# Optimization experiments

Hardware: AMD Instinct MI355X
Metric: run time of the kernel (lower is better)

Reference implementation:

```python
import jax, jax.numpy as jnp
import numpy as np

L = 3        # number of GatedGCN layers
N = 30000    # nodes
E = 480000   # edges (avg degree 16)
D = 128      # hidden dim (= in_dim = out_dim)
IN = 128     # input feature dim
G = 64       # graphs in batch
C = 10       # classes


def setup_inputs() -> dict:
    key = jax.random.key(0)
    ks = jax.random.split(key, 32)
    s = 0.05  # weight scale to keep activations / sigmoid gates in a sane range
    inp = {
        "h": jax.random.normal(ks[0], (N, IN), jnp.float32),
        "e": jax.random.normal(ks[1], (E, IN), jnp.float32),
        "snorm_n": jax.random.uniform(ks[2], (N, 1), jnp.float32),
        "snorm_e": jax.random.uniform(ks[3], (E, 1), jnp.float32),
        "src": jax.random.randint(ks[4], (E,), 0, N, jnp.int32),
        "dst": jax.random.randint(ks[5], (E,), 0, N, jnp.int32),
        "graph_id": jnp.sort(jax.random.randint(ks[6], (N,), 0, G, jnp.int32)),
        # input embeddings
        "Wh_emb": jax.random.normal(ks[7], (IN, D), jnp.float32) * s,
        "bh_emb": jnp.zeros((D,), jnp.float32),
        "We_emb": jax.random.normal(ks[8], (IN, D), jnp.float32) * s,
        "be_emb": jnp.zeros((D,), jnp.float32),
        # per-layer A,B,C,D,E linears (stacked over L)
        "WA": jax.random.normal(ks[9], (L, D, D), jnp.float32) * s,
        "bA": jnp.zeros((L, D), jnp.float32),
        "WB": jax.random.normal(ks[10], (L, D, D), jnp.float32) * s,
        "bB": jnp.zeros((L, D), jnp.float32),
        "WC": jax.random.normal(ks[11], (L, D, D), jnp.float32) * s,
        "bC": jnp.zeros((L, D), jnp.float32),
        "WD": jax.random.normal(ks[12], (L, D, D), jnp.float32) * s,
        "bD": jnp.zeros((L, D), jnp.float32),
        "WE": jax.random.normal(ks[13], (L, D, D), jnp.float32) * s,
        "bE": jnp.zeros((L, D), jnp.float32),
        # batch-norm affine params (node / edge)
        "gn_h": jnp.ones((L, D), jnp.float32),
        "bt_h": jnp.zeros((L, D), jnp.float32),
        "gn_e": jnp.ones((L, D), jnp.float32),
        "bt_e": jnp.zeros((L, D), jnp.float32),
        # readout linear
        "Wr": jax.random.normal(ks[14], (D, C), jnp.float32) * s,
        "br": jnp.zeros((C,), jnp.float32),
    }
    return inp


def _bn(x, gamma, beta):
    # training-mode BatchNorm1d: biased batch stats over the node/edge axis
    mu = jnp.mean(x, axis=0)
    var = jnp.var(x, axis=0)
    return (x - mu) * jax.lax.rsqrt(var + 1e-5) * gamma + beta


def reference(h, e, snorm_n, snorm_e, src, dst, graph_id,
              Wh_emb, bh_emb, We_emb, be_emb,
              WA, bA, WB, bB, WC, bC, WD, bD, WE, bE,
              gn_h, bt_h, gn_e, bt_e, Wr, br):
    n_nodes = h.shape[0]
    h = h @ Wh_emb + bh_emb
    e = e @ We_emb + be_emb
    for l in range(WA.shape[0]):
        h_in, e_in = h, e
        Ah = h @ WA[l] + bA[l]
        Bh = h @ WB[l] + bB[l]
        Dh = h @ WD[l] + bD[l]
        Eh = h @ WE[l] + bE[l]
        Ce = e @ WC[l] + bC[l]
        # message: e_ij = Ce + Dh_src + Eh_dst ; gate = sigmoid(e_ij)
        e_new = Ce + Dh[src] + Eh[dst]                       # [E, D]
        sig = jax.nn.sigmoid(e_new)
        # reduce at dst: gated weighted mean of Bh_src
        num = jax.ops.segment_sum(sig * Bh[src], dst, num_segments=n_nodes)
        den = jax.ops.segment_sum(sig, dst, num_segments=n_nodes)
        h_new = Ah + num / (den + 1e-6)
        # graph norm
        h_new = h_new * snorm_n
        e_new = e_new * snorm_e
        # batch norm + ReLU + residual (dropout p=0 -> identity)
        h_new = jax.nn.relu(_bn(h_new, gn_h[l], bt_h[l]))
        e_new = jax.nn.relu(_bn(e_new, gn_e[l], bt_e[l]))
        h = h_in + h_new
        e = e_in + e_new
    # mean_nodes readout per graph, then linear classifier
    sums = jax.ops.segment_sum(h, graph_id, num_segments=G)
    cnt = jax.ops.segment_sum(jnp.ones((n_nodes, 1), h.dtype), graph_id, num_segments=G)
    hg = sums / jnp.maximum(cnt, 1.0)
    return hg @ Wr + br
```

## Files before the change

### kernel.cpp

```cpp
#include <hip/hip_runtime.h>
#include <cstdint>
#include <cstddef>

#define N_NODES  30000
#define N_EDGES  480000
#define N_LAYERS 3
#define N_GRAPHS 64
#define N_CLASS  10
#define NREP     32

typedef __attribute__((ext_vector_type(8))) short short8v;
typedef __attribute__((ext_vector_type(4))) float f32x4;

__device__ __forceinline__ unsigned short f2bf(float x) {
  union { float f; unsigned u; } v; v.f = x;
  unsigned r = v.u + 0x7FFFu + ((v.u >> 16) & 1u);
  return (unsigned short)(r >> 16);
}
__device__ __forceinline__ float bf2f(unsigned short h) {
  union { unsigned u; float f; } v; v.u = ((unsigned)h) << 16;
  return v.f;
}
__device__ __forceinline__ int swzW(int row, int off16) {
  return (row << 8) | (off16 ^ ((row & 7) << 4));
}

__global__ void wconv(const float* __restrict__ Wh, const float* __restrict__ We,
                      const float* __restrict__ WA, const float* __restrict__ WB,
                      const float* __restrict__ WC, const float* __restrict__ WD,
                      const float* __restrict__ WE, unsigned short* __restrict__ Wt)
{
  const int mi  = blockIdx.x >> 6;
  const int idx = (blockIdx.x & 63) * 256 + threadIdx.x;
  const float* src;
  if      (mi == 0) src = Wh;
  else if (mi == 1) src = We;
  else if (mi < 5)  src = WA + (size_t)(mi - 2) * 16384;
  else if (mi < 8)  src = WB + (size_t)(mi - 5) * 16384;
  else if (mi < 11) src = WC + (size_t)(mi - 8) * 16384;
  else if (mi < 14) src = WD + (size_t)(mi - 11) * 16384;
  else              src = WE + (size_t)(mi - 14) * 16384;
  const int k = idx >> 7, n = idx & 127;
  Wt[(size_t)mi * 16384 + (size_t)n * 128 + k] = f2bf(src[idx]);
}

struct GemmArgs {
  const unsigned short* Wt[4];
  const float* bias[4];
  unsigned short* out[4];
};

template<int NMAT, bool AFP32, bool APPLY>
__global__ __launch_bounds__(256)
void gemm_mm(const void* __restrict__ Ap, GemmArgs g, int M,
             const float* __restrict__ tb, const float2* __restrict__ pqh,
             unsigned short* __restrict__ hout)
{
  __shared__ __align__(16) unsigned char WL[32768];
  unsigned short* Wl = (unsigned short*)WL;
  const int t = threadIdx.x;
  const int w = t >> 6, l = t & 63;
  const int lr = l & 15, lkb = (l >> 4) * 8;
  const int r0 = blockIdx.x * 64;
  const bool vrow = (r0 + w * 16 + lr) < M;
  int arow = r0 + w * 16 + lr; if (arow >= M) arow = M - 1;

  short8v a[4];
  if (AFP32) {
    const float* A = (const float*)Ap;
#pragma unroll
    for (int kk = 0; kk < 4; ++kk) {
      const float* p = A + (size_t)arow * 128 + kk * 32 + lkb;
      const float4 u = *(const float4*)p;
      const float4 v = *(const float4*)(p + 4);
      short8v av;
      av[0]=f2bf(u.x); av[1]=f2bf(u.y); av[2]=f2bf(u.z); av[3]=f2bf(u.w);
      av[4]=f2bf(v.x); av[5]=f2bf(v.y); av[6]=f2bf(v.z); av[7]=f2bf(v.w);
      a[kk] = av;
    }
  } else if (APPLY) {
    const unsigned short* A = (const unsigned short*)Ap;
#pragma unroll
    for (int kk = 0; kk < 4; ++kk) {
      const float* tp = tb + (size_t)arow * 128 + kk * 32 + lkb;
      const float4 t0 = *(const float4*)tp;
      const float4 t1 = *(const float4*)(tp + 4);
      const short8v hr = *(const short8v*)(A + (size_t)arow * 128 + kk * 32 + lkb);
      const float tt[8] = {t0.x,t0.y,t0.z,t0.w,t1.x,t1.y,t1.z,t1.w};
      short8v av;
#pragma unroll
      for (int j = 0; j < 8; ++j) {
        const float2 PQ = pqh[kk * 32 + lkb + j];
        const float x = tt[j] * PQ.x + PQ.y;
        av[j] = (short)f2bf(bf2f((unsigned short)hr[j]) + fmaxf(x, 0.f));
      }
      a[kk] = av;
      if (vrow) *(short8v*)(hout + (size_t)arow * 128 + kk * 32 + lkb) = av;
    }
  } else {
    const unsigned short* A = (const unsigned short*)Ap;
#pragma unroll
    for (int kk = 0; kk < 4; ++kk)
      a[kk] = *(const short8v*)(A + (size_t)arow * 128 + kk * 32 + lkb);
  }

#pragma unroll
  for (int m = 0; m < NMAT; ++m) {
    if (m) __syncthreads();
#pragma unroll
    for (int p = 0; p < 8; ++p) {
      const int ci = t + p * 256;
      *(short8v*)(WL + swzW(ci >> 4, (ci & 15) * 16)) = *(const short8v*)(g.Wt[m] + (size_t)ci * 8);
    }
    __syncthreads();
    f32x4 acc[8];
#pragma unroll
    for (int ct = 0; ct < 8; ++ct) acc[ct] = (f32x4){0.f, 0.f, 0.f, 0.f};
#pragma unroll
    for (int kk = 0; kk < 4; ++kk)
#pragma unroll
      for (int ct = 0; ct < 8; ++ct) {
        const short8v b = *(const short8v*)(WL + swzW(ct * 16 + lr, kk * 64 + (l >> 4) * 16));
        acc[ct] = __builtin_amdgcn_mfma_f32_16x16x32_bf16(a[kk], b, acc[ct], 0, 0, 0);
      }
    __syncthreads();
#pragma unroll
    for (int ct = 0; ct < 8; ++ct) {
      const float bb = g.bias[m][ct * 16 + lr];
#pragma unroll
      for (int q = 0; q < 4; ++q)
        Wl[(w * 16 + (l >> 4) * 4 + q) * 136 + ct * 16 + lr] = f2bf(acc[ct][q] + bb);
    }
    __syncthreads();
    unsigned short* out = g.out[m];
#pragma unroll
    for (int p = 0; p < 4; ++p) {
      const int ci = t + p * 256;
      const int rr = ci >> 4, co = (ci & 15) * 8;
      const int grow = r0 + rr;
      if (grow < M)
        *(short8v*)(out + (size_t)grow * 128 + co) = *(const short8v*)(Wl + rr * 136 + co);
    }
  }
}

template<int LMODE>
__global__ __launch_bounds__(256)
void edge_kern(const void* __restrict__ Ap, unsigned short* __restrict__ eres,
               unsigned short* __restrict__ enew,
               const unsigned short* __restrict__ Wt, const float* __restrict__ bias,
               const unsigned short* __restrict__ Dh, const unsigned short* __restrict__ Eh,
               const int* __restrict__ src, const int* __restrict__ dst,
               const float* __restrict__ snorm_e, const float2* __restrict__ pq)
{
  __shared__ __align__(16) unsigned char SM[33792];
  __shared__ float2 pql[128];
  unsigned short* TB = (unsigned short*)SM;
  const int t = threadIdx.x;
  const int w = t >> 6, l = t & 63;
  const int lr = l & 15, lkb = (l >> 4) * 8;
  const int r0 = blockIdx.x * 128;
  if (LMODE >= 2 && t < 128) pql[t] = pq[t];
#pragma unroll
  for (int p = 0; p < 8; ++p) {
    const int ci = t + p * 256;
    *(short8v*)(SM + swzW(ci >> 4, (ci & 15) * 16)) = *(const short8v*)(Wt + (size_t)ci * 8);
  }

  short8v a[2][4];
  if (LMODE == 0) {
    const float* A = (const float*)Ap;
#pragma unroll
    for (int mt = 0; mt < 2; ++mt) {
      const int arow = r0 + w * 32 + mt * 16 + lr;
#pragma unroll
      for (int kk = 0; kk < 4; ++kk) {
        const float* p2 = A + (size_t)arow * 128 + kk * 32 + lkb;
        const float4 u = *(const float4*)p2;
        const float4 v = *(const float4*)(p2 + 4);
        short8v av;
        av[0]=f2bf(u.x); av[1]=f2bf(u.y); av[2]=f2bf(u.z); av[3]=f2bf(u.w);
        av[4]=f2bf(v.x); av[5]=f2bf(v.y); av[6]=f2bf(v.z); av[7]=f2bf(v.w);
        a[mt][kk] = av;
      }
    }
  } else if (LMODE == 1) {
    const unsigned short* A = (const unsigned short*)Ap;
#pragma unroll
    for (int mt = 0; mt < 2; ++mt) {
      const int arow = r0 + w * 32 + mt * 16 + lr;
#pragma unroll
      for (int kk = 0; kk < 4; ++kk)
        a[mt][kk] = *(const short8v*)(A + (size_t)arow * 128 + kk * 32 + lkb);
    }
  }
  __syncthreads();

  if (LMODE >= 2) {
    const unsigned short* A = (const unsigned short*)Ap;
#pragma unroll
    for (int mt = 0; mt < 2; ++mt) {
      const int arow = r0 + w * 32 + mt * 16 + lr;
      const float sn = snorm_e[arow];
#pragma unroll
      for (int kk = 0; kk < 4; ++kk) {
        const short8v ep = *(const short8v*)(enew + (size_t)arow * 128 + kk * 32 + lkb);
        const short8v er = *(const short8v*)(A + (size_t)arow * 128 + kk * 32 + lkb);
        short8v av;
#pragma unroll
        for (int j = 0; j < 8; ++j) {
          const float2 PQ = pql[kk * 32 + lkb + j];
          const float x = bf2f((unsigned short)ep[j]) * sn * PQ.x + PQ.y;
          av[j] = (short)f2bf(bf2f((unsigned short)er[j]) + fmaxf(x, 0.f));
        }
        a[mt][kk] = av;
        if (LMODE == 2)
          *(short8v*)(eres + (size_t)arow * 128 + kk * 32 + lkb) = av;
      }
    }
  }

  f32x4 acc[2][8];
#pragma unroll
  for (int mt = 0; mt < 2; ++mt)
#pragma unroll
    for (int ct = 0; ct < 8; ++ct) acc[mt][ct] = (f32x4){0.f, 0.f, 0.f, 0.f};
#pragma unroll
  for (int kk = 0; kk < 4; ++kk)
#pragma unroll
    for (int ct = 0; ct < 8; ++ct) {
      const short8v b = *(const short8v*)(SM + swzW(ct * 16 + lr, kk * 64 + (l >> 4) * 16));
      acc[0][ct] = __builtin_amdgcn_mfma_f32_16x16x32_bf16(a[0][kk], b, acc[0][ct], 0, 0, 0);
      acc[1][ct] = __builtin_amdgcn_mfma_f32_16x16x32_bf16(a[1][kk], b, acc[1][ct], 0, 0, 0);
    }
  __syncthreads();
#pragma unroll
  for (int ct = 0; ct < 8; ++ct) {
    const float bb = bias[ct * 16 + lr];
#pragma unroll
    for (int mt = 0; mt < 2; ++mt)
#pragma unroll
      for (int q = 0; q < 4; ++q)
        TB[(w * 32 + mt * 16 + (l >> 4) * 4 + q) * 132 + ct * 16 + lr] = f2bf(acc[mt][ct][q] + bb);
  }
  __syncthreads();
#pragma unroll
  for (int p = 0; p < 8; ++p) {
    const int ci = t + p * 256;
    const int rr = ci >> 4, co = (ci & 15) * 8;
    const int edge = r0 + rr;
    const short8v ce = *(const short8v*)(TB + rr * 132 + co);
    if (LMODE == 0) {
      *(short8v*)(eres + (size_t)edge * 128 + co) = ce;
    } else {
      const int s = src[edge], d = dst[edge];
      const short8v dv = *(const short8v*)(Dh + (size_t)s * 128 + co);
      const short8v ev = *(const short8v*)(Eh + (size_t)d * 128 + co);
      short8v ov;
#pragma unroll
      for (int j = 0; j < 8; ++j)
        ov[j] = (short)f2bf(bf2f((unsigned short)ce[j]) + bf2f((unsigned short)dv[j]) + bf2f((unsigned short)ev[j]));
      *(short8v*)(enew + (size_t)edge * 128 + co) = ov;
    }
  }
}

__global__ void hist_kernel(const int* __restrict__ dst, int* __restrict__ cnt, int E)
{
  const int i = blockIdx.x * 256 + threadIdx.x;
  if (i < E) atomicAdd(&cnt[dst[i]], 1);
}

__global__ void scan_kernel(const int* __restrict__ cnt, int* __restrict__ start,
                            int* __restrict__ cursor, int n, int total)
{
  __shared__ int lds[1024];
  const int tid = threadIdx.x;
  const int chunk = (n + 1023) / 1024;
  const int lo = tid * chunk, hi = min(lo + chunk, n);
  int s = 0;
  for (int i = lo; i < hi; ++i) s += cnt[i];
  lds[tid] = s;
  __syncthreads();
  for (int off = 1; off < 1024; off <<= 1) {
    const int v = (tid >= off) ? lds[tid - off] : 0;
    __syncthreads();
    lds[tid] += v;
    __syncthreads();
  }
  int run = (tid == 0) ? 0 : lds[tid - 1];
  for (int i = lo; i < hi; ++i) { start[i] = run; cursor[i] = run; run += cnt[i]; }
  if (tid == 0) start[n] = total;
}

__global__ void scatter_kernel(const int* __restrict__ dst, const int* __restrict__ src,
                               const float* __restrict__ sne, int* __restrict__ cursor,
                               int* __restrict__ csr, int* __restrict__ csrc,
                               float* __restrict__ csne, int E)
{
  const int i = blockIdx.x * 256 + threadIdx.x;
  if (i < E) {
    const int p = atomicAdd(&cursor[dst[i]], 1);
    csr[p] = i; csrc[p] = src[i]; csne[p] = sne[i];
  }
}

__global__ __launch_bounds__(256)
void aggregate(const unsigned short* __restrict__ enew, const unsigned short* __restrict__ Bh,
               const unsigned short* __restrict__ Ah, const float* __restrict__ snorm_n,
               const int* __restrict__ start, const int* __restrict__ csr,
               const int* __restrict__ csrc, const float* __restrict__ csne,
               float* __restrict__ tbuf, float* __restrict__ statrep, int doE)
{
  __shared__ float2 red[16][132];
  const int t = threadIdx.x;
  const int g = t >> 4, q = t & 15;
  const int v = blockIdx.x * 16 + g;
  const int s0 = start[v], s1 = start[v + 1];
  float num[8] = {0,0,0,0,0,0,0,0}, den[8] = {0,0,0,0,0,0,0,0};
  float psE[8] = {0,0,0,0,0,0,0,0}, pqE[8] = {0,0,0,0,0,0,0,0};

  float sn = 0.f;
  short8v ev = {}, bv = {};
  if (s0 < s1) {
    const int eid = csr[s0];
    sn = csne[s0];
    ev = *(const short8v*)(enew + (size_t)eid * 128 + q * 8);
    bv = *(const short8v*)(Bh + (size_t)csrc[s0] * 128 + q * 8);
  }
  for (int i = s0; i < s1; ++i) {
    float snn = 0.f;
    short8v evn = {}, bvn = {};
    if (i + 1 < s1) {
      const int eid = csr[i + 1];
      snn = csne[i + 1];
      evn = *(const short8v*)(enew + (size_t)eid * 128 + q * 8);
      bvn = *(const short8v*)(Bh + (size_t)csrc[i + 1] * 128 + q * 8);
    }
#pragma unroll
    for (int j = 0; j < 8; ++j) {
      const float en = bf2f((unsigned short)ev[j]);
      const float sg = 1.f / (1.f + __expf(-en));
      num[j] = fmaf(sg, bf2f((unsigned short)bv[j]), num[j]);
      den[j] += sg;
      if (doE) { const float tv = en * sn; psE[j] += tv; pqE[j] = fmaf(tv, tv, pqE[j]); }
    }
    ev = evn; bv = bvn; sn = snn;
  }
  const float snv = snorm_n[v];
  const short8v av = *(const short8v*)(Ah + (size_t)v * 128 + q * 8);
  float hv[8];
#pragma unroll
  for (int j = 0; j < 8; ++j)
    hv[j] = (bf2f((unsigned short)av[j]) + num[j] / (den[j] + 1e-6f)) * snv;
  *(float4*)(tbuf + (size_t)v * 128 + q * 8)     = make_float4(hv[0], hv[1], hv[2], hv[3]);
  *(float4*)(tbuf + (size_t)v * 128 + q * 8 + 4) = make_float4(hv[4], hv[5], hv[6], hv[7]);

  float* rep = statrep + (size_t)(blockIdx.x & (NREP - 1)) * 512;
#pragma unroll
  for (int j = 0; j < 8; ++j) red[g][q * 8 + j] = make_float2(hv[j], hv[j] * hv[j]);
  __syncthreads();
  if (t < 128) {
    float s = 0.f, qq = 0.f;
    for (int gg = 0; gg < 16; ++gg) { s += red[gg][t].x; qq += red[gg][t].y; }
    atomicAdd(rep + t, s); atomicAdd(rep + 128 + t, qq);
  }
  if (doE) {
    __syncthreads();
#pragma unroll
    for (int j = 0; j < 8; ++j) red[g][q * 8 + j] = make_float2(psE[j], pqE[j]);
    __syncthreads();
    if (t < 128) {
      float s = 0.f, qq = 0.f;
      for (int gg = 0; gg < 16; ++gg) { s += red[gg][t].x; qq += red[gg][t].y; }
      atomicAdd(rep + 256 + t, s); atomicAdd(rep + 384 + t, qq);
    }
  }
}

__global__ void finalize_kernel(float* __restrict__ rep, float2* __restrict__ pqh,
                                float2* __restrict__ pqe,
                                const float* __restrict__ gn_h_l, const float* __restrict__ bt_h_l,
                                const float* __restrict__ gn_e_l, const float* __restrict__ bt_e_l,
                                float invN, float invE, int doE)
{
  const int c = threadIdx.x;
  float sH = 0.f, qH = 0.f, sE = 0.f, qE = 0.f;
  for (int r = 0; r < NREP; ++r) {
    float* p = rep + (size_t)r * 512;
    sH += p[c]; qH += p[128 + c]; sE += p[256 + c]; qE += p[384 + c];
    p[c] = 0.f; p[128 + c] = 0.f; p[256 + c] = 0.f; p[384 + c] = 0.f;
  }
  const float muH = sH * invN;
  const float vH  = fmaxf(qH * invN - muH * muH, 0.f);
  const float PH  = rsqrtf(vH + 1e-5f) * gn_h_l[c];
  pqh[c] = make_float2(PH, bt_h_l[c] - muH * PH);
  if (doE) {
    const float muE = sE * invE;
    const float vE  = fmaxf(qE * invE - muE * muE, 0.f);
    const float PE  = rsqrtf(vE + 1e-5f) * gn_e_l[c];
    pqe[c] = make_float2(PE, bt_e_l[c] - muE * PE);
  }
}

__global__ void readout_scatter(const unsigned short* __restrict__ h, const float* __restrict__ tb,
                                const float2* __restrict__ pqh, const int* __restrict__ gid,
                                float* __restrict__ gsum, int* __restrict__ gcnt, int N)
{
  const int c = threadIdx.x;
  const float2 PQ = pqh[c];
  const int row0 = blockIdx.x * 256;
  int cur = -1, cnt = 0;
  float s = 0.f;
  for (int r = 0; r < 256; ++r) {
    const int v = row0 + r;
    if (v >= N) break;
    const int g = gid[v];
    if (g != cur) {
      if (cur >= 0) {
        atomicAdd(&gsum[(size_t)cur * 128 + c], s);
        if (c == 0) atomicAdd(&gcnt[cur], cnt);
      }
      cur = g; s = 0.f; cnt = 0;
    }
    s += bf2f(h[(size_t)v * 128 + c]) + fmaxf(tb[(size_t)v * 128 + c] * PQ.x + PQ.y, 0.f);
    ++cnt;
  }
  if (cur >= 0) {
    atomicAdd(&gsum[(size_t)cur * 128 + c], s);
    if (c == 0) atomicAdd(&gcnt[cur], cnt);
  }
}

__global__ void readout_final(const float* __restrict__ gsum, const int* __restrict__ gcnt,
                              const float* __restrict__ Wr, const float* __restrict__ br,
                              float* __restrict__ out)
{
  const int g = blockIdx.x;
  const int t = threadIdx.x;
  __shared__ float hg[128];
  const float cnt = fmaxf((float)gcnt[g], 1.f);
  hg[t] = gsum[(size_t)g * 128 + t] / cnt;
  __syncthreads();
  if (t < N_CLASS) {
    float acc = br[t];
    for (int k = 0; k < 128; ++k) acc = fmaf(hg[k], Wr[k * N_CLASS + t], acc);
    out[g * N_CLASS + t] = acc;
  }
}

extern "C" void kernel_launch(void* const* d_in, const int* in_sizes, int n_in,
                              void* d_out, int out_size, void* d_ws, size_t ws_size,
                              hipStream_t stream)
{
  const float* h_in    = (const float*)d_in[0];
  const float* e_in    = (const float*)d_in[1];
  const float* snorm_n = (const float*)d_in[2];
  const float* snorm_e = (const float*)d_in[3];
  const int*   src     = (const int*)d_in[4];
  const int*   dst     = (const int*)d_in[5];
  const int*   gid     = (const int*)d_in[6];
  const float* Wh_emb  = (const float*)d_in[7];
  const float* bh_emb  = (const float*)d_in[8];
  const float* We_emb  = (const float*)d_in[9];
  const float* be_emb  = (const float*)d_in[10];
  const float* WA = (const float*)d_in[11]; const float* bA = (const float*)d_in[12];
  const float* WB = (const float*)d_in[13]; const float* bB = (const float*)d_in[14];
  const float* WC = (const float*)d_in[15]; const float* bC = (const float*)d_in[16];
  const float* WD = (const float*)d_in[17]; const float* bD = (const float*)d_in[18];
  const float* WE = (const float*)d_in[19]; const float* bE = (const float*)d_in[20];
  const float* gn_h = (const float*)d_in[21]; const float* bt_h = (const float*)d_in[22];
  const float* gn_e = (const float*)d_in[23]; const float* bt_e = (const float*)d_in[24];
  const float* Wr = (const float*)d_in[25]; const float* br = (const float*)d_in[26];
  float* out = (float*)d_out;
  (void)in_sizes; (void)n_in; (void)out_size; (void)ws_size;

  char* ws = (char*)d_ws;
  size_t off = 0;
  auto alloc = [&](size_t bytes) -> char* {
    off = (off + 255) & ~(size_t)255;
    char* p = ws + off;
    off += bytes;
    return p;
  };
  const size_t ND = (size_t)N_NODES * 128, ED = (size_t)N_EDGES * 128;
  unsigned short* hbuf = (unsigned short*)alloc(ND * 2);
  unsigned short* ebuf = (unsigned short*)alloc(ED * 2);
  unsigned short* enew = (unsigned short*)alloc(ED * 2);
  unsigned short* Ah   = (unsigned short*)alloc(ND * 2);
  unsigned short* Bh   = (unsigned short*)alloc(ND * 2);
  unsigned short* Dh   = (unsigned short*)alloc(ND * 2);
  unsigned short* Eh   = (unsigned short*)alloc(ND * 2);
  float* tbuf          = (float*)alloc(ND * 4);
  unsigned short* Wt   = (unsigned short*)alloc((size_t)17 * 16384 * 2);
  float* statrep       = (float*)alloc((size_t)NREP * 512 * 4);
  float2* pqh          = (float2*)alloc(128 * 8);
  float2* pqe          = (float2*)alloc(128 * 8);
  int* cnt    = (int*)alloc((size_t)N_NODES * 4);
  int* start  = (int*)alloc((size_t)(N_NODES + 1) * 4);
  int* cursor = (int*)alloc((size_t)N_NODES * 4);
  int* csr    = (int*)alloc((size_t)N_EDGES * 4);
  int* csrc   = (int*)alloc((size_t)N_EDGES * 4);
  float* csne = (float*)alloc((size_t)N_EDGES * 4);
  float* gsum = (float*)alloc((size_t)N_GRAPHS * 128 * 4);
  int* gcnt   = (int*)alloc((size_t)N_GRAPHS * 4);

  wconv<<<17 * 64, 256, 0, stream>>>(Wh_emb, We_emb, WA, WB, WC, WD, WE, Wt);

  hipMemsetAsync(cnt, 0, (size_t)N_NODES * 4, stream);
  hipMemsetAsync(statrep, 0, (size_t)NREP * 512 * 4, stream);
  hist_kernel<<<(N_EDGES + 255) / 256, 256, 0, stream>>>(dst, cnt, N_EDGES);
  scan_kernel<<<1, 1024, 0, stream>>>(cnt, start, cursor, N_NODES, N_EDGES);
  scatter_kernel<<<(N_EDGES + 255) / 256, 256, 0, stream>>>(dst, src, snorm_e, cursor,
                                                            csr, csrc, csne, N_EDGES);

  const int gbN = (N_NODES + 63) / 64;
  const int gbE = N_EDGES / 128;

  {
    GemmArgs g{};
    g.Wt[0] = Wt + 0 * 16384; g.bias[0] = bh_emb; g.out[0] = hbuf;
    gemm_mm<1, true, false><<<gbN, 256, 0, stream>>>(h_in, g, N_NODES, nullptr, nullptr, nullptr);
  }
  edge_kern<0><<<gbE, 256, 0, stream>>>(e_in, ebuf, nullptr, Wt + 1 * 16384, be_emb,
                                        nullptr, nullptr, nullptr, nullptr, nullptr, nullptr);

  for (int l = 0; l < N_LAYERS; ++l) {
    const size_t bOff = (size_t)l * 128;
    const int doE = (l < N_LAYERS - 1) ? 1 : 0;
    {
      GemmArgs g{};
      g.Wt[0] = Wt + (size_t)(2 + l)  * 16384; g.bias[0] = bA + bOff; g.out[0] = Ah;
      g.Wt[1] = Wt + (size_t)(5 + l)  * 16384; g.bias[1] = bB + bOff; g.out[1] = Bh;
      g.Wt[2] = Wt + (size_t)(11 + l) * 16384; g.bias[2] = bD + bOff; g.out[2] = Dh;
      g.Wt[3] = Wt + (size_t)(14 + l) * 16384; g.bias[3] = bE + bOff; g.out[3] = Eh;
      if (l == 0)
        gemm_mm<4, false, false><<<gbN, 256, 0, stream>>>(hbuf, g, N_NODES, nullptr, nullptr, nullptr);
      else
        gemm_mm<4, false, true><<<gbN, 256, 0, stream>>>(hbuf, g, N_NODES, tbuf, pqh, hbuf);
    }
    const unsigned short* WtC = Wt + (size_t)(8 + l) * 16384;
    if (l == 0)
      edge_kern<1><<<gbE, 256, 0, stream>>>(ebuf, nullptr, enew, WtC, bC + bOff,
                                            Dh, Eh, src, dst, nullptr, nullptr);
    else if (l == 1)
      edge_kern<2><<<gbE, 256, 0, stream>>>(ebuf, ebuf, enew, WtC, bC + bOff,
                                            Dh, Eh, src, dst, snorm_e, pqe);
    else
      edge_kern<3><<<gbE, 256, 0, stream>>>(ebuf, nullptr, enew, WtC, bC + bOff,
                                            Dh, Eh, src, dst, snorm_e, pqe);
    aggregate<<<N_NODES / 16, 256, 0, stream>>>(enew, Bh, Ah, snorm_n,
                                                start, csr, csrc, csne, tbuf, statrep, doE);
    finalize_kernel<<<1, 128, 0, stream>>>(statrep, pqh, pqe, gn_h + bOff, bt_h + bOff,
                                           gn_e + bOff, bt_e + bOff,
                                           1.f / N_NODES, 1.f / N_EDGES, doE);
  }

  hipMemsetAsync(gsum, 0, (size_t)N_GRAPHS * 128 * 4 + (size_t)N_GRAPHS * 4, stream);
  readout_scatter<<<(N_NODES + 255) / 256, 128, 0, stream>>>(hbuf, tbuf, pqh, gid, gsum, gcnt, N_NODES);
  readout_final<<<N_GRAPHS, 128, 0, stream>>>(gsum, gcnt, Wr, br, out);
}
```

Before: 984.9 us.

## Fuse BN finalize into aggregate, store node pre-norm in bf16, shrink edge tiles

```diff
diff --git a/kernel.cpp b/kernel.cpp
--- a/kernel.cpp
+++ b/kernel.cpp
@@ -53,7 +53,7 @@
 template<int NMAT, bool AFP32, bool APPLY>
 __global__ __launch_bounds__(256)
 void gemm_mm(const void* __restrict__ Ap, GemmArgs g, int M,
-             const float* __restrict__ tb, const float2* __restrict__ pqh,
+             const unsigned short* __restrict__ tb, const float2* __restrict__ pqh,
              unsigned short* __restrict__ hout)
 {
   __shared__ __align__(16) unsigned char WL[32768];
@@ -82,16 +82,13 @@
     const unsigned short* A = (const unsigned short*)Ap;
 #pragma unroll
     for (int kk = 0; kk < 4; ++kk) {
-      const float* tp = tb + (size_t)arow * 128 + kk * 32 + lkb;
-      const float4 t0 = *(const float4*)tp;
-      const float4 t1 = *(const float4*)(tp + 4);
+      const short8v tv = *(const short8v*)(tb + (size_t)arow * 128 + kk * 32 + lkb);
       const short8v hr = *(const short8v*)(A + (size_t)arow * 128 + kk * 32 + lkb);
-      const float tt[8] = {t0.x,t0.y,t0.z,t0.w,t1.x,t1.y,t1.z,t1.w};
       short8v av;
 #pragma unroll
       for (int j = 0; j < 8; ++j) {
         const float2 PQ = pqh[kk * 32 + lkb + j];
-        const float x = tt[j] * PQ.x + PQ.y;
+        const float x = bf2f((unsigned short)tv[j]) * PQ.x + PQ.y;
         av[j] = (short)f2bf(bf2f((unsigned short)hr[j]) + fmaxf(x, 0.f));
       }
       a[kk] = av;
@@ -153,13 +150,14 @@
                const int* __restrict__ src, const int* __restrict__ dst,
                const float* __restrict__ snorm_e, const float2* __restrict__ pq)
 {
-  __shared__ __align__(16) unsigned char SM[33792];
+  __shared__ __align__(16) unsigned char SM[32768];
   __shared__ float2 pql[128];
   unsigned short* TB = (unsigned short*)SM;
   const int t = threadIdx.x;
   const int w = t >> 6, l = t & 63;
   const int lr = l & 15, lkb = (l >> 4) * 8;
-  const int r0 = blockIdx.x * 128;
+  const int r0 = blockIdx.x * 64;
+  const int arow = r0 + w * 16 + lr;
   if (LMODE >= 2 && t < 128) pql[t] = pq[t];
 #pragma unroll
   for (int p = 0; p < 8; ++p) {
@@ -167,85 +165,68 @@
     *(short8v*)(SM + swzW(ci >> 4, (ci & 15) * 16)) = *(const short8v*)(Wt + (size_t)ci * 8);
   }
 
-  short8v a[2][4];
+  short8v a[4];
   if (LMODE == 0) {
     const float* A = (const float*)Ap;
 #pragma unroll
-    for (int mt = 0; mt < 2; ++mt) {
-      const int arow = r0 + w * 32 + mt * 16 + lr;
-#pragma unroll
-      for (int kk = 0; kk < 4; ++kk) {
-        const float* p2 = A + (size_t)arow * 128 + kk * 32 + lkb;
-        const float4 u = *(const float4*)p2;
-        const float4 v = *(const float4*)(p2 + 4);
-        short8v av;
-        av[0]=f2bf(u.x); av[1]=f2bf(u.y); av[2]=f2bf(u.z); av[3]=f2bf(u.w);
-        av[4]=f2bf(v.x); av[5]=f2bf(v.y); av[6]=f2bf(v.z); av[7]=f2bf(v.w);
-        a[mt][kk] = av;
-      }
+    for (int kk = 0; kk < 4; ++kk) {
+      const float* p2 = A + (size_t)arow * 128 + kk * 32 + lkb;
+      const float4 u = *(const float4*)p2;
+      const float4 v = *(const float4*)(p2 + 4);
+      short8v av;
+      av[0]=f2bf(u.x); av[1]=f2bf(u.y); av[2]=f2bf(u.z); av[3]=f2bf(u.w);
+      av[4]=f2bf(v.x); av[5]=f2bf(v.y); av[6]=f2bf(v.z); av[7]=f2bf(v.w);
+      a[kk] = av;
     }
   } else if (LMODE == 1) {
     const unsigned short* A = (const unsigned short*)Ap;
 #pragma unroll
-    for (int mt = 0; mt < 2; ++mt) {
-      const int arow = r0 + w * 32 + mt * 16 + lr;
-#pragma unroll
-      for (int kk = 0; kk < 4; ++kk)
-        a[mt][kk] = *(const short8v*)(A + (size_t)arow * 128 + kk * 32 + lkb);
-    }
+    for (int kk = 0; kk < 4; ++kk)
+      a[kk] = *(const short8v*)(A + (size_t)arow * 128 + kk * 32 + lkb);
   }
   __syncthreads();
 
   if (LMODE >= 2) {
     const unsigned short* A = (const unsigned short*)Ap;
-#pragma unroll
-    for (int mt = 0; mt < 2; ++mt) {
-      const int arow = r0 + w * 32 + mt * 16 + lr;
-      const float sn = snorm_e[arow];
-#pragma unroll
-      for (int kk = 0; kk < 4; ++kk) {
-        const short8v ep = *(const short8v*)(enew + (size_t)arow * 128 + kk * 32 + lkb);
-        const short8v er = *(const short8v*)(A + (size_t)arow * 128 + kk * 32 + lkb);
-        short8v av;
-#pragma unroll
-        for (int j = 0; j < 8; ++j) {
-          const float2 PQ = pql[kk * 32 + lkb + j];
-          const float x = bf2f((unsigned short)ep[j]) * sn * PQ.x + PQ.y;
-          av[j] = (short)f2bf(bf2f((unsigned short)er[j]) + fmaxf(x, 0.f));
-        }
-        a[mt][kk] = av;
-        if (LMODE == 2)
-          *(short8v*)(eres + (size_t)arow * 128 + kk * 32 + lkb) = av;
+    const float sn = snorm_e[arow];
+#pragma unroll
+    for (int kk = 0; kk < 4; ++kk) {
+      const short8v ep = *(const short8v*)(enew + (size_t)arow * 128 + kk * 32 + lkb);
+      const short8v er = *(const short8v*)(A + (size_t)arow * 128 + kk * 32 + lkb);
+      short8v av;
+#pragma unroll
+      for (int j = 0; j < 8; ++j) {
+        const float2 PQ = pql[kk * 32 + lkb + j];
+        const float x = bf2f((unsigned short)ep[j]) * sn * PQ.x + PQ.y;
+        av[j] = (short)f2bf(bf2f((unsigned short)er[j]) + fmaxf(x, 0.f));
       }
-    }
-  }
-
-  f32x4 acc[2][8];
-#pragma unroll
-  for (int mt = 0; mt < 2; ++mt)
-#pragma unroll
-    for (int ct = 0; ct < 8; ++ct) acc[mt][ct] = (f32x4){0.f, 0.f, 0.f, 0.f};
+      a[kk] = av;
+      if (LMODE == 2)
+        *(short8v*)(eres + (size_t)arow * 128 + kk * 32 + lkb) = av;
+    }
+  }
+
+  f32x4 acc[8];
+#pragma unroll
+  for (int ct = 0; ct < 8; ++ct) acc[ct] = (f32x4){0.f, 0.f, 0.f, 0.f};
 #pragma unroll
   for (int kk = 0; kk < 4; ++kk)
 #pragma unroll
     for (int ct = 0; ct < 8; ++ct) {
       const short8v b = *(const short8v*)(SM + swzW(ct * 16 + lr, kk * 64 + (l >> 4) * 16));
-      acc[0][ct] = __builtin_amdgcn_mfma_f32_16x16x32_bf16(a[0][kk], b, acc[0][ct], 0, 0, 0);
-      acc[1][ct] = __builtin_amdgcn_mfma_f32_16x16x32_bf16(a[1][kk], b, acc[1][ct], 0, 0, 0);
+      acc[ct] = __builtin_amdgcn_mfma_f32_16x16x32_bf16(a[kk], b, acc[ct], 0, 0, 0);
     }
   __syncthreads();
 #pragma unroll
   for (int ct = 0; ct < 8; ++ct) {
     const float bb = bias[ct * 16 + lr];
 #pragma unroll
-    for (int mt = 0; mt < 2; ++mt)
-#pragma unroll
-      for (int q = 0; q < 4; ++q)
-        TB[(w * 32 + mt * 16 + (l >> 4) * 4 + q) * 132 + ct * 16 + lr] = f2bf(acc[mt][ct][q] + bb);
-  }
-  __syncthreads();
-#pragma unroll
-  for (int p = 0; p < 8; ++p) {
+    for (int q = 0; q < 4; ++q)
+      TB[(w * 16 + (l >> 4) * 4 + q) * 132 + ct * 16 + lr] = f2bf(acc[ct][q] + bb);
+  }
+  __syncthreads();
+#pragma unroll
+  for (int p = 0; p < 4; ++p) {
     const int ci = t + p * 256;
     const int rr = ci >> 4, co = (ci & 15) * 8;
     const int edge = r0 + rr;
@@ -305,14 +286,19 @@
   }
 }
 
+template<int DOE>
 __global__ __launch_bounds__(256)
 void aggregate(const unsigned short* __restrict__ enew, const unsigned short* __restrict__ Bh,
                const unsigned short* __restrict__ Ah, const float* __restrict__ snorm_n,
                const int* __restrict__ start, const int* __restrict__ csr,
                const int* __restrict__ csrc, const float* __restrict__ csne,
-               float* __restrict__ tbuf, float* __restrict__ statrep, int doE)
+               unsigned short* __restrict__ tbuf, float* __restrict__ statrep,
+               int* __restrict__ ticket, float2* __restrict__ pqh, float2* __restrict__ pqe,
+               const float* __restrict__ gn_h_l, const float* __restrict__ bt_h_l,
+               const float* __restrict__ gn_e_l, const float* __restrict__ bt_e_l)
 {
   __shared__ float2 red[16][132];
+  __shared__ int lastF;
   const int t = threadIdx.x;
   const int g = t >> 4, q = t & 15;
   const int v = blockIdx.x * 16 + g;
@@ -343,18 +329,20 @@
       const float sg = 1.f / (1.f + __expf(-en));
       num[j] = fmaf(sg, bf2f((unsigned short)bv[j]), num[j]);
       den[j] += sg;
-      if (doE) { const float tv = en * sn; psE[j] += tv; pqE[j] = fmaf(tv, tv, pqE[j]); }
+      if (DOE) { const float tv = en * sn; psE[j] += tv; pqE[j] = fmaf(tv, tv, pqE[j]); }
     }
     ev = evn; bv = bvn; sn = snn;
   }
   const float snv = snorm_n[v];
   const short8v av = *(const short8v*)(Ah + (size_t)v * 128 + q * 8);
   float hv[8];
-#pragma unroll
-  for (int j = 0; j < 8; ++j)
+  short8v tout;
+#pragma unroll
+  for (int j = 0; j < 8; ++j) {
     hv[j] = (bf2f((unsigned short)av[j]) + num[j] / (den[j] + 1e-6f)) * snv;
-  *(float4*)(tbuf + (size_t)v * 128 + q * 8)     = make_float4(hv[0], hv[1], hv[2], hv[3]);
-  *(float4*)(tbuf + (size_t)v * 128 + q * 8 + 4) = make_float4(hv[4], hv[5], hv[6], hv[7]);
+    tout[j] = (short)f2bf(hv[j]);
+  }
+  *(short8v*)(tbuf + (size_t)v * 128 + q * 8) = tout;
 
   float* rep = statrep + (size_t)(blockIdx.x & (NREP - 1)) * 512;
 #pragma unroll
@@ -365,7 +353,7 @@
     for (int gg = 0; gg < 16; ++gg) { s += red[gg][t].x; qq += red[gg][t].y; }
     atomicAdd(rep + t, s); atomicAdd(rep + 128 + t, qq);
   }
-  if (doE) {
+  if (DOE) {
     __syncthreads();
 #pragma unroll
     for (int j = 0; j < 8; ++j) red[g][q * 8 + j] = make_float2(psE[j], pqE[j]);
@@ -376,34 +364,37 @@
       atomicAdd(rep + 256 + t, s); atomicAdd(rep + 384 + t, qq);
     }
   }
-}
-
-__global__ void finalize_kernel(float* __restrict__ rep, float2* __restrict__ pqh,
-                                float2* __restrict__ pqe,
-                                const float* __restrict__ gn_h_l, const float* __restrict__ bt_h_l,
-                                const float* __restrict__ gn_e_l, const float* __restrict__ bt_e_l,
-                                float invN, float invE, int doE)
-{
-  const int c = threadIdx.x;
-  float sH = 0.f, qH = 0.f, sE = 0.f, qE = 0.f;
-  for (int r = 0; r < NREP; ++r) {
-    float* p = rep + (size_t)r * 512;
-    sH += p[c]; qH += p[128 + c]; sE += p[256 + c]; qE += p[384 + c];
-    p[c] = 0.f; p[128 + c] = 0.f; p[256 + c] = 0.f; p[384 + c] = 0.f;
-  }
-  const float muH = sH * invN;
-  const float vH  = fmaxf(qH * invN - muH * muH, 0.f);
-  const float PH  = rsqrtf(vH + 1e-5f) * gn_h_l[c];
-  pqh[c] = make_float2(PH, bt_h_l[c] - muH * PH);
-  if (doE) {
-    const float muE = sE * invE;
-    const float vE  = fmaxf(qE * invE - muE * muE, 0.f);
-    const float PE  = rsqrtf(vE + 1e-5f) * gn_e_l[c];
-    pqe[c] = make_float2(PE, bt_e_l[c] - muE * PE);
-  }
-}
-
-__global__ void readout_scatter(const unsigned short* __restrict__ h, const float* __restrict__ tb,
+  __threadfence();
+  __syncthreads();
+  if (t == 0) lastF = (atomicAdd(ticket, 1) == (int)gridDim.x - 1) ? 1 : 0;
+  __syncthreads();
+  if (lastF) {
+    __threadfence();
+    if (t < 128) {
+      const int c = t;
+      float sH = 0.f, qH = 0.f, sE = 0.f, qE = 0.f;
+      for (int r = 0; r < NREP; ++r) {
+        volatile float* p = statrep + (size_t)r * 512;
+        sH += p[c]; qH += p[128 + c];
+        if (DOE) { sE += p[256 + c]; qE += p[384 + c]; }
+        p[c] = 0.f; p[128 + c] = 0.f; p[256 + c] = 0.f; p[384 + c] = 0.f;
+      }
+      const float invN = 1.f / N_NODES, invE = 1.f / N_EDGES;
+      const float muH = sH * invN;
+      const float vH  = fmaxf(qH * invN - muH * muH, 0.f);
+      const float PH  = rsqrtf(vH + 1e-5f) * gn_h_l[c];
+      pqh[c] = make_float2(PH, bt_h_l[c] - muH * PH);
+      if (DOE) {
+        const float muE = sE * invE;
+        const float vE  = fmaxf(qE * invE - muE * muE, 0.f);
+        const float PE  = rsqrtf(vE + 1e-5f) * gn_e_l[c];
+        pqe[c] = make_float2(PE, bt_e_l[c] - muE * PE);
+      }
+    }
+  }
+}
+
+__global__ void readout_scatter(const unsigned short* __restrict__ h, const unsigned short* __restrict__ tb,
                                 const float2* __restrict__ pqh, const int* __restrict__ gid,
                                 float* __restrict__ gsum, int* __restrict__ gcnt, int N)
 {
@@ -423,7 +414,7 @@
       }
       cur = g; s = 0.f; cnt = 0;
     }
-    s += bf2f(h[(size_t)v * 128 + c]) + fmaxf(tb[(size_t)v * 128 + c] * PQ.x + PQ.y, 0.f);
+    s += bf2f(h[(size_t)v * 128 + c]) + fmaxf(bf2f(tb[(size_t)v * 128 + c]) * PQ.x + PQ.y, 0.f);
     ++cnt;
   }
   if (cur >= 0) {
@@ -491,31 +482,34 @@
   unsigned short* Bh   = (unsigned short*)alloc(ND * 2);
   unsigned short* Dh   = (unsigned short*)alloc(ND * 2);
   unsigned short* Eh   = (unsigned short*)alloc(ND * 2);
-  float* tbuf          = (float*)alloc(ND * 4);
+  unsigned short* tbuf = (unsigned short*)alloc(ND * 2);
   unsigned short* Wt   = (unsigned short*)alloc((size_t)17 * 16384 * 2);
-  float* statrep       = (float*)alloc((size_t)NREP * 512 * 4);
   float2* pqh          = (float2*)alloc(128 * 8);
   float2* pqe          = (float2*)alloc(128 * 8);
-  int* cnt    = (int*)alloc((size_t)N_NODES * 4);
   int* start  = (int*)alloc((size_t)(N_NODES + 1) * 4);
   int* cursor = (int*)alloc((size_t)N_NODES * 4);
   int* csr    = (int*)alloc((size_t)N_EDGES * 4);
   int* csrc   = (int*)alloc((size_t)N_EDGES * 4);
   float* csne = (float*)alloc((size_t)N_EDGES * 4);
-  float* gsum = (float*)alloc((size_t)N_GRAPHS * 128 * 4);
-  int* gcnt   = (int*)alloc((size_t)N_GRAPHS * 4);
+  char* zbase = (char*)alloc(0);
+  int*   cnt     = (int*)alloc((size_t)N_NODES * 4);
+  float* statrep = (float*)alloc((size_t)NREP * 512 * 4);
+  float* gsum    = (float*)alloc((size_t)N_GRAPHS * 128 * 4);
+  int*   gcnt    = (int*)alloc((size_t)N_GRAPHS * 4);
+  int*   tickets = (int*)alloc(8 * 4);
+  char* zend = (char*)alloc(0);
+
+  hipMemsetAsync(zbase, 0, (size_t)(zend - zbase), stream);
 
   wconv<<<17 * 64, 256, 0, stream>>>(Wh_emb, We_emb, WA, WB, WC, WD, WE, Wt);
 
-  hipMemsetAsync(cnt, 0, (size_t)N_NODES * 4, stream);
-  hipMemsetAsync(statrep, 0, (size_t)NREP * 512 * 4, stream);
   hist_kernel<<<(N_EDGES + 255) / 256, 256, 0, stream>>>(dst, cnt, N_EDGES);
   scan_kernel<<<1, 1024, 0, stream>>>(cnt, start, cursor, N_NODES, N_EDGES);
   scatter_kernel<<<(N_EDGES + 255) / 256, 256, 0, stream>>>(dst, src, snorm_e, cursor,
                                                             csr, csrc, csne, N_EDGES);
 
   const int gbN = (N_NODES + 63) / 64;
-  const int gbE = N_EDGES / 128;
+  const int gbE = N_EDGES / 64;
 
   {
     GemmArgs g{};
@@ -527,7 +521,6 @@
 
   for (int l = 0; l < N_LAYERS; ++l) {
     const size_t bOff = (size_t)l * 128;
-    const int doE = (l < N_LAYERS - 1) ? 1 : 0;
     {
       GemmArgs g{};
       g.Wt[0] = Wt + (size_t)(2 + l)  * 16384; g.bias[0] = bA + bOff; g.out[0] = Ah;
@@ -549,14 +542,16 @@
     else
       edge_kern<3><<<gbE, 256, 0, stream>>>(ebuf, nullptr, enew, WtC, bC + bOff,
                                             Dh, Eh, src, dst, snorm_e, pqe);
-    aggregate<<<N_NODES / 16, 256, 0, stream>>>(enew, Bh, Ah, snorm_n,
-                                                start, csr, csrc, csne, tbuf, statrep, doE);
-    finalize_kernel<<<1, 128, 0, stream>>>(statrep, pqh, pqe, gn_h + bOff, bt_h + bOff,
-                                           gn_e + bOff, bt_e + bOff,
-                                           1.f / N_NODES, 1.f / N_EDGES, doE);
-  }
-
-  hipMemsetAsync(gsum, 0, (size_t)N_GRAPHS * 128 * 4 + (size_t)N_GRAPHS * 4, stream);
+    if (l < N_LAYERS - 1)
+      aggregate<1><<<N_NODES / 16, 256, 0, stream>>>(enew, Bh, Ah, snorm_n, start, csr, csrc, csne,
+                                                     tbuf, statrep, tickets + l, pqh, pqe,
+                                                     gn_h + bOff, bt_h + bOff, gn_e + bOff, bt_e + bOff);
+    else
+      aggregate<0><<<N_NODES / 16, 256, 0, stream>>>(enew, Bh, Ah, snorm_n, start, csr, csrc, csne,
+                                                     tbuf, statrep, tickets + l, pqh, pqe,
+                                                     gn_h + bOff, bt_h + bOff, gn_e + bOff, bt_e + bOff);
+  }
+
   readout_scatter<<<(N_NODES + 255) / 256, 128, 0, stream>>>(hbuf, tbuf, pqh, gid, gsum, gcnt, N_NODES);
   readout_final<<<N_GRAPHS, 128, 0, stream>>>(gsum, gcnt, Wr, br, out);
 }
```

New measurement: 1.681 ms. 1.71x slower.
